# Kernel tuning notes

Measured on AMD Instinct MI355X. Metric: run time of the kernel, lower is better.

The kernel has to match this reference:

```python
import jax, jax.numpy as jnp
import numpy as np

NH = 16   # neighbors
MD = 64   # model_dim
FF = 128  # ff_dim
H = 4     # heads
HD = MD // H
B, S, T = 2, 8192, 4096
LOG100 = float(np.log(100.0))


def _ln(x, g, b, eps=1e-5):
    m = x.mean(-1, keepdims=True)
    v = ((x - m) ** 2).mean(-1, keepdims=True)
    return (x - m) * jax.lax.rsqrt(v + eps) * g + b


def _lrelu(x):
    return jnp.where(x >= 0, x, 0.2 * x)


def setup_inputs():
    ks = jax.random.split(jax.random.key(0), 16)
    rn = lambda k, sh: jax.random.normal(k, sh, dtype=jnp.float32) * 0.05
    return {
        "x": jax.random.normal(ks[0], (B, S, 1), dtype=jnp.float32),
        "c1": jax.random.normal(ks[1], (B, S, T), dtype=jnp.float32),
        "c2": jax.random.normal(ks[2], (B, S, T), dtype=jnp.float32),
        "pe_W1": rn(ks[3], (2, FF)), "pe_b1": jnp.zeros((FF,), jnp.float32),
        "pe_W2": rn(ks[4], (FF, MD)), "pe_b2": jnp.zeros((MD,), jnp.float32),
        "Wq": rn(ks[5], (MD, MD)), "Wk": rn(ks[6], (MD, MD)), "Wv": rn(ks[7], (1, MD)),
        "logit_scale": jnp.full((H, 1, 1), float(np.log(10.0)), jnp.float32),
        "Wo": rn(ks[8], (MD, MD)), "bo": jnp.zeros((MD,), jnp.float32),
        "g1": jnp.ones((MD,), jnp.float32), "beta1": jnp.zeros((MD,), jnp.float32),
        "g2": jnp.ones((MD,), jnp.float32), "beta2": jnp.zeros((MD,), jnp.float32),
        "g3": jnp.ones((MD * NH,), jnp.float32), "beta3": jnp.zeros((MD * NH,), jnp.float32),
        "mnh_W1": rn(ks[9], (MD, FF)), "mnh_b1": jnp.zeros((FF,), jnp.float32),
        "mnh_W2": rn(ks[10], (FF, 1)), "mnh_b2": jnp.zeros((1,), jnp.float32),
        "mu_W1": rn(ks[11], (MD * NH, MD * NH)), "mu_b1": jnp.zeros((MD * NH,), jnp.float32),
        "mu_W2": rn(ks[12], (MD * NH, MD * NH)), "mu_b2": jnp.zeros((MD * NH,), jnp.float32),
    }


def reference(x, c1, c2, pe_W1, pe_b1, pe_W2, pe_b2, Wq, Wk, Wv, logit_scale, Wo, bo,
              g1, beta1, g2, beta2, g3, beta3,
              mnh_W1, mnh_b1, mnh_W2, mnh_b2, mu_W1, mu_b1, mu_W2, mu_b2):
    b, s, t = c1.shape
    # KNN over source axis s (cartesian distance), per target t
    d = c1 * c1 + c2 * c2                                  # [b,s,t]
    _, idx = jax.lax.top_k(-jnp.swapaxes(d, 1, 2), NH)     # [b,t,NH]
    x_nh = jax.vmap(lambda xb, ib: xb[ib])(x, idx)         # [b,t,NH,e]
    c1g = jnp.take_along_axis(jnp.swapaxes(c1, 1, 2), idx, axis=2)  # [b,t,NH]
    c2g = jnp.take_along_axis(jnp.swapaxes(c2, 1, 2), idx, axis=2)
    # relative-position embedding MLP (PE), already in [b,t,NH,MD] layout
    pe = jnp.stack([c1g, c2g], -1)                         # [b,t,NH,2]
    pe = jax.nn.gelu(pe @ pe_W1 + pe_b1) @ pe_W2 + pe_b2   # [b,t,NH,MD]
    h = _ln(x_nh + pe, g1, beta1).reshape(b * t, NH, MD)   # e=1 broadcasts
    v = jnp.einsum('bne,ed->bnd', x_nh.reshape(b * t, NH, 1), Wv)
    q = h @ Wq
    k = h @ Wk
    sp = lambda z: z.reshape(b * t, NH, H, HD).transpose(0, 2, 1, 3)
    qh, kh, vh = sp(q), sp(k), sp(v)
    # logit-scaled (cosine) attention over the NH neighbor axis
    qn = qh * jax.lax.rsqrt(jnp.sum(qh * qh, -1, keepdims=True) + 1e-12)
    kn = kh * jax.lax.rsqrt(jnp.sum(kh * kh, -1, keepdims=True) + 1e-12)
    scale = jnp.exp(jnp.minimum(logit_scale, LOG100))      # [H,1,1]
    att = jax.nn.softmax(jnp.einsum('bhnd,bhmd->bhnm', qn, kn) * scale, axis=-1)
    o = jnp.einsum('bhnm,bhmd->bhnd', att, vh).transpose(0, 2, 1, 3).reshape(b * t, NH, MD)
    h = _ln(h + (o @ Wo + bo), g2, beta2)
    # per-neighbor MLP producing a scalar, broadcast-added back
    h = h + _lrelu(_lrelu(h @ mnh_W1 + mnh_b1) @ mnh_W2 + mnh_b2)
    # unfold neighbors into channels and run the unfold MLP
    h = _ln(h.reshape(b, t, NH * MD), g3, beta3)
    return _lrelu(_lrelu(h @ mu_W1 + mu_b1) @ mu_W2 + mu_b2)  # [b,t,NH*MD]
```

## Files before the change

kernel.cpp:

```cpp
#include <hip/hip_runtime.h>
#include <hip/hip_bf16.h>

#define B_    2
#define SSRC  8192
#define TT    4096
#define NHN   16
#define NC    64
#define CS    128
#define LOG100D 4.605170185988091368035982909368

typedef short s16x8 __attribute__((ext_vector_type(8)));
typedef float f32x4 __attribute__((ext_vector_type(4)));
typedef unsigned long long u64;

typedef const __attribute__((address_space(1))) void* gas_ptr;
typedef __attribute__((address_space(3))) void* las_ptr;
#define GLDS16(g, l) __builtin_amdgcn_global_load_lds((gas_ptr)(g), (las_ptr)(l), 16, 0, 0)

#define WFENCE asm volatile("s_waitcnt lgkmcnt(0)" ::: "memory")

__device__ __forceinline__ unsigned short f2bf(float f) {
    unsigned u = __float_as_uint(f);
    u = u + 0x7fffu + ((u >> 16) & 1u);
    return (unsigned short)(u >> 16);
}
__device__ __forceinline__ float bf2f(unsigned short h) {
    return __uint_as_float(((unsigned)h) << 16);
}
__device__ __forceinline__ double lrelu_d(double v) { return v >= 0.0 ? v : 0.2 * v; }
__device__ __forceinline__ double gelu_d(double u) {
    double a = 0.7978845608028654 * (u + 0.044715 * u * u * u);
    return 0.5 * u * (1.0 + tanh(a));
}
__device__ __forceinline__ double rsum16d(double v) {
    v += __shfl_xor(v, 1); v += __shfl_xor(v, 2);
    v += __shfl_xor(v, 4); v += __shfl_xor(v, 8);
    return v;
}
__device__ __forceinline__ double rmax16d(double v) {
    v = fmax(v, __shfl_xor(v, 1)); v = fmax(v, __shfl_xor(v, 2));
    v = fmax(v, __shfl_xor(v, 4)); v = fmax(v, __shfl_xor(v, 8));
    return v;
}
__device__ __forceinline__ double rsum64d(double v) {
    v += __shfl_xor(v, 1); v += __shfl_xor(v, 2); v += __shfl_xor(v, 4);
    v += __shfl_xor(v, 8); v += __shfl_xor(v, 16); v += __shfl_xor(v, 32);
    return v;
}

__device__ __forceinline__ void ce(u64 &a, u64 &b) {
    bool c = a < b; u64 lo = c ? a : b; u64 hi = c ? b : a; a = lo; b = hi;
}
__device__ __forceinline__ void sort16(u64 (&k)[16]) {
    ce(k[0],k[8]); ce(k[1],k[9]); ce(k[2],k[10]); ce(k[3],k[11]);
    ce(k[4],k[12]); ce(k[5],k[13]); ce(k[6],k[14]); ce(k[7],k[15]);
    ce(k[0],k[4]); ce(k[1],k[5]); ce(k[2],k[6]); ce(k[3],k[7]);
    ce(k[8],k[12]); ce(k[9],k[13]); ce(k[10],k[14]); ce(k[11],k[15]);
    ce(k[4],k[8]); ce(k[5],k[9]); ce(k[6],k[10]); ce(k[7],k[11]);
    ce(k[0],k[2]); ce(k[1],k[3]); ce(k[4],k[6]); ce(k[5],k[7]);
    ce(k[8],k[10]); ce(k[9],k[11]); ce(k[12],k[14]); ce(k[13],k[15]);
    ce(k[2],k[8]); ce(k[3],k[9]); ce(k[6],k[12]); ce(k[7],k[13]);
    ce(k[2],k[4]); ce(k[3],k[5]); ce(k[6],k[8]); ce(k[7],k[9]);
    ce(k[10],k[12]); ce(k[11],k[13]);
    ce(k[0],k[1]); ce(k[2],k[3]); ce(k[4],k[5]); ce(k[6],k[7]);
    ce(k[8],k[9]); ce(k[10],k[11]); ce(k[12],k[13]); ce(k[14],k[15]);
    ce(k[1],k[8]); ce(k[3],k[10]); ce(k[5],k[12]); ce(k[7],k[14]);
    ce(k[1],k[4]); ce(k[3],k[6]); ce(k[5],k[8]); ce(k[7],k[10]);
    ce(k[9],k[12]); ce(k[11],k[14]);
    ce(k[1],k[2]); ce(k[3],k[4]); ce(k[5],k[6]); ce(k[7],k[8]);
    ce(k[9],k[10]); ce(k[11],k[12]); ce(k[13],k[14]);
}
__device__ __forceinline__ void bmerge16(u64 (&k)[16]) {
    ce(k[0],k[8]); ce(k[1],k[9]); ce(k[2],k[10]); ce(k[3],k[11]);
    ce(k[4],k[12]); ce(k[5],k[13]); ce(k[6],k[14]); ce(k[7],k[15]);
    ce(k[0],k[4]); ce(k[1],k[5]); ce(k[2],k[6]); ce(k[3],k[7]);
    ce(k[8],k[12]); ce(k[9],k[13]); ce(k[10],k[14]); ce(k[11],k[15]);
    ce(k[0],k[2]); ce(k[1],k[3]); ce(k[4],k[6]); ce(k[5],k[7]);
    ce(k[8],k[10]); ce(k[9],k[11]); ce(k[12],k[14]); ce(k[13],k[15]);
    ce(k[0],k[1]); ce(k[2],k[3]); ce(k[4],k[5]); ce(k[6],k[7]);
    ce(k[8],k[9]); ce(k[10],k[11]); ce(k[12],k[13]); ce(k[14],k[15]);
}
__device__ __forceinline__ void merge_keep16(u64 (&L)[16], const u64 (&B)[16]) {
#pragma unroll
    for (int i = 0; i < 16; i++) { u64 bb = B[15 - i]; L[i] = L[i] < bb ? L[i] : bb; }
    bmerge16(L);
}

__global__ __launch_bounds__(256) void topk_partial(
    const float* __restrict__ c1, const float* __restrict__ c2,
    u64* __restrict__ cand)
{
    int t = blockIdx.x * 256 + threadIdx.x;
    int ch = blockIdx.y, b = blockIdx.z;
    const float* p1 = c1 + ((size_t)b * SSRC + (size_t)ch * CS) * TT + t;
    const float* p2 = c2 + ((size_t)b * SSRC + (size_t)ch * CS) * TT + t;
    u64 k[16];
#pragma unroll
    for (int j = 0; j < 16; j++) k[j] = ~0ull;
    int sbase = ch * CS;
    for (int s = 0; s < CS; s += 16) {
        u64 bt[16];
#pragma unroll
        for (int u = 0; u < 16; u++) {
            float a_ = p1[(size_t)(s + u) * TT];
            float b_ = p2[(size_t)(s + u) * TT];
            float dd = __fadd_rn(__fmul_rn(a_, a_), __fmul_rn(b_, b_));
            bt[u] = ((u64)__float_as_uint(dd) << 32) | (unsigned)(sbase + s + u);
        }
        sort16(bt);
        merge_keep16(k, bt);
    }
    u64* dst = cand + ((size_t)(b * NC + ch) * 16) * TT + t;
#pragma unroll
    for (int j = 0; j < 16; j++) dst[(size_t)j * TT] = k[j];
}

__global__ __launch_bounds__(64) void topk_merge1(
    const u64* __restrict__ cand, u64* __restrict__ c2c)
{
    int t = blockIdx.x * 64 + threadIdx.x;
    int g = blockIdx.y, b = blockIdx.z;
    u64 k[16];
#pragma unroll
    for (int j = 0; j < 16; j++) k[j] = ~0ull;
    for (int c = g * 8; c < g * 8 + 8; c++) {
        const u64* src = cand + ((size_t)(b * NC + c) * 16) * TT + t;
        u64 bt[16];
#pragma unroll
        for (int j = 0; j < 16; j++) bt[j] = src[(size_t)j * TT];
        merge_keep16(k, bt);
    }
    u64* dst = c2c + ((size_t)((b * 8 + g) * 16)) * TT + t;
#pragma unroll
    for (int j = 0; j < 16; j++) dst[(size_t)j * TT] = k[j];
}

__global__ __launch_bounds__(64) void topk_merge2(
    const u64* __restrict__ c2c, int* __restrict__ knn)
{
    int t = blockIdx.x * 64 + threadIdx.x;
    int b = blockIdx.y;
    u64 k[16];
#pragma unroll
    for (int j = 0; j < 16; j++) k[j] = ~0ull;
    for (int c = 0; c < 8; c++) {
        const u64* src = c2c + ((size_t)(b * 8 + c) * 16) * TT + t;
        u64 bt[16];
#pragma unroll
        for (int j = 0; j < 16; j++) bt[j] = src[(size_t)j * TT];
        merge_keep16(k, bt);
    }
#pragma unroll
    for (int j = 0; j < 16; j++)
        knn[((size_t)b * TT + t) * 16 + j] = (int)(unsigned)(k[j] & 0xffffffffull);
}

__global__ __launch_bounds__(256) void wconv(
    const float* __restrict__ Wa, const float* __restrict__ Wb,
    unsigned short* __restrict__ Oah, unsigned short* __restrict__ Oal,
    unsigned short* __restrict__ Obh, unsigned short* __restrict__ Obl)
{
    const float* W = blockIdx.z ? Wb : Wa;
    unsigned short* Oh = blockIdx.z ? Obh : Oah;
    unsigned short* Ol = blockIdx.z ? Obl : Oal;
    __shared__ float tile[64][65];
    int tx = threadIdx.x & 63, ty = threadIdx.x >> 6;
    int n0 = blockIdx.x * 64, k0 = blockIdx.y * 64;
#pragma unroll
    for (int r = ty; r < 64; r += 4) tile[r][tx] = W[(size_t)(k0 + r) * 1024 + n0 + tx];
    __syncthreads();
#pragma unroll
    for (int r = ty; r < 64; r += 4) {
        float v = tile[tx][r];
        unsigned short hi = f2bf(v);
        Oh[(size_t)(n0 + r) * 1024 + k0 + tx] = hi;
        Ol[(size_t)(n0 + r) * 1024 + k0 + tx] = f2bf(v - bf2f(hi));
    }
}

__global__ __launch_bounds__(256) void tok_pe(
    const float* __restrict__ x, const float* __restrict__ c1, const float* __restrict__ c2,
    const int* __restrict__ knn,
    const float* __restrict__ peW1, const float* __restrict__ peb1,
    const float* __restrict__ peW2, const float* __restrict__ peb2,
    const float* __restrict__ g1, const float* __restrict__ be1,
    float* __restrict__ hout)
{
    __shared__ float s_peW1[256], s_peb1[128], s_peW2[8192], s_peb2[64], s_g1[64], s_be1[64];
    __shared__ float s_scr[4][2352];
    int tid = threadIdx.x, lane = tid & 63, w = tid >> 6;
    if (tid < 256) s_peW1[tid] = peW1[tid];
    if (tid < 128) s_peb1[tid] = peb1[tid];
    if (tid < 64) { s_peb2[tid] = peb2[tid]; s_g1[tid] = g1[tid]; s_be1[tid] = be1[tid]; }
    for (int i = tid; i < 8192; i += 256) s_peW2[i] = peW2[i];
    __syncthreads();

    float* big = s_scr[w];
    float* sc1 = big + 2304; float* sc2 = big + 2320; float* sx = big + 2336;
    double w0a = s_peW1[lane], w1a = s_peW1[128 + lane], ba = s_peb1[lane];
    double w0b = s_peW1[64 + lane], w1b = s_peW1[192 + lane], bbv = s_peb1[64 + lane];
    double gv = (double)s_g1[lane], bv = (double)s_be1[lane];
    double pb2 = (double)s_peb2[lane];

    for (int it = 0; it < 4; ++it) {
        int tk = blockIdx.x * 16 + w * 4 + it;
        int bb = tk >> 12, tt = tk & (TT - 1);
        if (lane < 16) {
            int s = knn[(size_t)tk * 16 + lane];
            sc1[lane] = c1[((size_t)bb * SSRC + s) * TT + tt];
            sc2[lane] = c2[((size_t)bb * SSRC + s) * TT + tt];
            sx[lane]  = x[bb * SSRC + s];
        }
        WFENCE;
#pragma unroll
        for (int n = 0; n < 16; n++) {
            double a_ = (double)sc1[n], b_ = (double)sc2[n];
            big[lane * 18 + n]        = (float)gelu_d(a_ * w0a + b_ * w1a + ba);
            big[(lane + 64) * 18 + n] = (float)gelu_d(a_ * w0b + b_ * w1b + bbv);
        }
        WFENCE;
        double acc[16];
#pragma unroll
        for (int n = 0; n < 16; n++) acc[n] = pb2;
        for (int f = 0; f < 128; f++) {
            double wv = (double)s_peW2[f * 64 + lane];
#pragma unroll
            for (int n = 0; n < 16; n += 2) {
                float2 gvv = *(const float2*)&big[f * 18 + n];
                acc[n]     += (double)gvv.x * wv;
                acc[n + 1] += (double)gvv.y * wv;
            }
        }
        float* op = hout + (size_t)tk * 1024 + lane;
#pragma unroll
        for (int n = 0; n < 16; n++) {
            double v = acc[n] + (double)sx[n];
            double m = rsum64d(v) * (1.0 / 64.0);
            double d = v - m;
            double var = rsum64d(d * d) * (1.0 / 64.0);
            op[n * 64] = (float)(d / sqrt(var + 1e-5) * gv + bv);
        }
    }
}

__global__ __launch_bounds__(256) void tok_attn(
    const float* __restrict__ x, const int* __restrict__ knn,
    const float* __restrict__ Wq, const float* __restrict__ Wk,
    const float* __restrict__ Wv, const float* __restrict__ lsc,
    const float* __restrict__ Wo, const float* __restrict__ bo,
    const float* __restrict__ g2, const float* __restrict__ be2,
    float* __restrict__ hio)
{
    __shared__ float s_Wq[4096], s_Wk[4096], s_WoV[256], s_bo[64], s_g2[64], s_be2[64];
    __shared__ float s_scr[4][2320];
    int tid = threadIdx.x, lane = tid & 63, w = tid >> 6;
    if (tid < 64) {
        s_bo[tid] = bo[tid]; s_g2[tid] = g2[tid]; s_be2[tid] = be2[tid];
        for (int hh = 0; hh < 4; hh++) {
            double a = 0.0;
            for (int hd = 0; hd < 16; hd++)
                a += (double)Wv[hh * 16 + hd] * (double)Wo[(hh * 16 + hd) * 64 + tid];
            s_WoV[hh * 64 + tid] = (float)a;
        }
    }
    for (int i = tid; i < 4096; i += 256) { s_Wq[i] = Wq[i]; s_Wk[i] = Wk[i]; }
    __syncthreads();

    int head = lane >> 4, mm = lane & 15;
    double scaleh = exp(fmin((double)lsc[head], LOG100D));
    double wov0 = (double)s_WoV[lane], wov1 = (double)s_WoV[64 + lane];
    double wov2 = (double)s_WoV[128 + lane], wov3 = (double)s_WoV[192 + lane];
    double gv = (double)s_g2[lane], bv = (double)s_be2[lane], bov = (double)s_bo[lane];
    float* big = s_scr[w];
    float* sx = big + 2304;

    for (int it = 0; it < 4; ++it) {
        int tk = blockIdx.x * 16 + w * 4 + it;
        int bb = tk >> 12;
        if (lane < 16) {
            int s = knn[(size_t)tk * 16 + lane];
            sx[lane] = x[bb * SSRC + s];
        }
        float* hp = hio + (size_t)tk * 1024 + lane;
        double h[16];
#pragma unroll
        for (int n = 0; n < 16; n++) {
            h[n] = (double)hp[n * 64];
            big[lane * 18 + n] = (float)h[n];
        }
        WFENCE;
        double q[16], k2[16];
#pragma unroll
        for (int n = 0; n < 16; n++) { q[n] = 0.0; k2[n] = 0.0; }
        for (int kk = 0; kk < 64; kk++) {
            double wq = (double)s_Wq[kk * 64 + lane], wk = (double)s_Wk[kk * 64 + lane];
#pragma unroll
            for (int n = 0; n < 16; n += 2) {
                float2 hv = *(const float2*)&big[kk * 18 + n];
                q[n]  += (double)hv.x * wq; q[n + 1]  += (double)hv.y * wq;
                k2[n] += (double)hv.x * wk; k2[n + 1] += (double)hv.y * wk;
            }
        }
#pragma unroll
        for (int n = 0; n < 16; n++) {
            double sq = rsum16d(q[n] * q[n]);   q[n]  /= sqrt(sq + 1e-12);
            double sk = rsum16d(k2[n] * k2[n]); k2[n] /= sqrt(sk + 1e-12);
        }
        WFENCE;
#pragma unroll
        for (int n = 0; n < 16; n++) {
            big[lane * 18 + n]        = (float)q[n];
            big[1152 + lane * 18 + n] = (float)k2[n];
        }
        WFENCE;
        double A_[16];
        {
            double S[16];
#pragma unroll
            for (int n = 0; n < 16; n++) S[n] = 0.0;
            for (int hd = 0; hd < 16; hd++) {
                int r = head * 16 + hd;
                double kf = (double)big[1152 + r * 18 + mm];
#pragma unroll
                for (int n = 0; n < 16; n += 2) {
                    float2 qq = *(const float2*)&big[r * 18 + n];
                    S[n] += (double)qq.x * kf; S[n + 1] += (double)qq.y * kf;
                }
            }
            double xv = (double)sx[mm];
#pragma unroll
            for (int n = 0; n < 16; n++) {
                double sv = S[n] * scaleh;
                double mx = rmax16d(sv);
                double e = exp(sv - mx);
                double se = rsum16d(e);
                A_[n] = rsum16d((e / se) * xv);
            }
        }
#pragma unroll
        for (int n = 0; n < 16; n++) {
            double a0 = __shfl(A_[n], mm), a1 = __shfl(A_[n], 16 + mm);
            double a2 = __shfl(A_[n], 32 + mm), a3 = __shfl(A_[n], 48 + mm);
            double v = h[n] + a0 * wov0 + a1 * wov1 + a2 * wov2 + a3 * wov3 + bov;
            double m = rsum64d(v) * (1.0 / 64.0);
            double d = v - m;
            double var = rsum64d(d * d) * (1.0 / 64.0);
            hp[n * 64] = (float)(d / sqrt(var + 1e-5) * gv + bv);
        }
    }
}

__global__ __launch_bounds__(256) void tok_mnh(
    const float* __restrict__ hin,
    const float* __restrict__ mW1, const float* __restrict__ mb1,
    const float* __restrict__ mW2, const float* __restrict__ mb2,
    const float* __restrict__ g3, const float* __restrict__ be3,
    unsigned short* __restrict__ hnh, unsigned short* __restrict__ hnl)
{
    __shared__ float s_mW1[8192], s_mb1[128], s_mW2[128], s_g3[1024], s_be3[1024];
    __shared__ float s_scr[4][1152];
    int tid = threadIdx.x, lane = tid & 63, w = tid >> 6;
    if (tid < 128) { s_mb1[tid] = mb1[tid]; s_mW2[tid] = mW2[tid]; }
    for (int i = tid; i < 8192; i += 256) s_mW1[i] = mW1[i];
    for (int i = tid; i < 1024; i += 256) { s_g3[i] = g3[i]; s_be3[i] = be3[i]; }
    __syncthreads();

    double mb2s = (double)mb2[0];
    double mb1a = (double)s_mb1[lane], mb1b = (double)s_mb1[64 + lane];
    double w2a = (double)s_mW2[lane], w2b = (double)s_mW2[64 + lane];
    float* big = s_scr[w];

    for (int it = 0; it < 4; ++it) {
        int tk = blockIdx.x * 16 + w * 4 + it;
        const float* hp = hin + (size_t)tk * 1024 + lane;
        double h[16];
#pragma unroll
        for (int n = 0; n < 16; n++) {
            h[n] = (double)hp[n * 64];
            big[lane * 18 + n] = (float)h[n];
        }
        WFENCE;
        double t1a[16], t1b[16];
#pragma unroll
        for (int n = 0; n < 16; n++) { t1a[n] = mb1a; t1b[n] = mb1b; }
        for (int kk = 0; kk < 64; kk++) {
            double wa = (double)s_mW1[kk * 128 + lane], wb = (double)s_mW1[kk * 128 + 64 + lane];
#pragma unroll
            for (int n = 0; n < 16; n += 2) {
                float2 hv = *(const float2*)&big[kk * 18 + n];
                t1a[n] += (double)hv.x * wa; t1a[n + 1] += (double)hv.y * wa;
                t1b[n] += (double)hv.x * wb; t1b[n + 1] += (double)hv.y * wb;
            }
        }
#pragma unroll
        for (int n = 0; n < 16; n++) {
            double p = lrelu_d(t1a[n]) * w2a + lrelu_d(t1b[n]) * w2b;
            p = rsum64d(p);
            h[n] += lrelu_d(p + mb2s);
        }
        double s1 = 0.0;
#pragma unroll
        for (int n = 0; n < 16; n++) s1 += h[n];
        s1 = rsum64d(s1) * (1.0 / 1024.0);
        double s2v = 0.0;
#pragma unroll
        for (int n = 0; n < 16; n++) { double d = h[n] - s1; s2v += d * d; }
        s2v = rsum64d(s2v) * (1.0 / 1024.0);
        double rs = 1.0 / sqrt(s2v + 1e-5);
        unsigned short* oph = hnh + (size_t)tk * 1024 + lane;
        unsigned short* opl = hnl + (size_t)tk * 1024 + lane;
#pragma unroll
        for (int n = 0; n < 16; n++) {
            double v = (h[n] - s1) * rs * (double)s_g3[n * 64 + lane] + (double)s_be3[n * 64 + lane];
            unsigned short hi = f2bf((float)v);
            oph[n * 64] = hi;
            opl[n * 64] = f2bf((float)(v - (double)bf2f(hi)));
        }
    }
}

#define AH_OFF 0
#define AL_OFF 4096
#define BH_OFF 8192
#define BL_OFF 12288
template<int OUTSPLIT>
__global__ __launch_bounds__(256) void gemm_split(
    const unsigned short* __restrict__ Ah, const unsigned short* __restrict__ Al,
    const unsigned short* __restrict__ Bh, const unsigned short* __restrict__ Bl,
    const float* __restrict__ bias,
    unsigned short* __restrict__ oh, unsigned short* __restrict__ ol,
    float* __restrict__ of, int M, int N, int K)
{
    __shared__ unsigned short SM[16384];
    int tid = threadIdx.x, lane = tid & 63, w = tid >> 6;
    int wm = w >> 1, wn = w & 1;
    int m0 = blockIdx.y * 128, n0 = blockIdx.x * 128;
    f32x4 acc[4][4];
#pragma unroll
    for (int i = 0; i < 4; i++)
#pragma unroll
        for (int j = 0; j < 4; j++) acc[i][j] = (f32x4){0.f, 0.f, 0.f, 0.f};
    int row = tid >> 2, c8 = (tid & 3) * 8;
    size_t aoff = (size_t)(m0 + row) * K + c8;
    size_t boff = (size_t)(n0 + row) * K + c8;
    for (int kk = 0; kk < K; kk += 32) {
        __syncthreads();
        GLDS16(Ah + aoff + kk,                   SM + AH_OFF + tid * 8);
        GLDS16(Ah + aoff + (size_t)64 * K + kk,  SM + AH_OFF + 2048 + tid * 8);
        GLDS16(Al + aoff + kk,                   SM + AL_OFF + tid * 8);
        GLDS16(Al + aoff + (size_t)64 * K + kk,  SM + AL_OFF + 2048 + tid * 8);
        GLDS16(Bh + boff + kk,                   SM + BH_OFF + tid * 8);
        GLDS16(Bh + boff + (size_t)64 * K + kk,  SM + BH_OFF + 2048 + tid * 8);
        GLDS16(Bl + boff + kk,                   SM + BL_OFF + tid * 8);
        GLDS16(Bl + boff + (size_t)64 * K + kk,  SM + BL_OFF + 2048 + tid * 8);
        asm volatile("s_waitcnt vmcnt(0)" ::: "memory");
        __syncthreads();
        int kh = (lane >> 4) * 8, rA = wm * 64 + (lane & 15), rB = wn * 64 + (lane & 15);
        s16x8 afh[4], afl[4], bfh[4], bfl[4];
#pragma unroll
        for (int i = 0; i < 4; i++) {
            afh[i] = *(const s16x8*)&SM[AH_OFF + (rA + i * 16) * 32 + kh];
            afl[i] = *(const s16x8*)&SM[AL_OFF + (rA + i * 16) * 32 + kh];
            bfh[i] = *(const s16x8*)&SM[BH_OFF + (rB + i * 16) * 32 + kh];
            bfl[i] = *(const s16x8*)&SM[BL_OFF + (rB + i * 16) * 32 + kh];
        }
#pragma unroll
        for (int i = 0; i < 4; i++)
#pragma unroll
            for (int j = 0; j < 4; j++) {
                acc[i][j] = __builtin_amdgcn_mfma_f32_16x16x32_bf16(afl[i], bfh[j], acc[i][j], 0, 0, 0);
                acc[i][j] = __builtin_amdgcn_mfma_f32_16x16x32_bf16(afh[i], bfl[j], acc[i][j], 0, 0, 0);
                acc[i][j] = __builtin_amdgcn_mfma_f32_16x16x32_bf16(afh[i], bfh[j], acc[i][j], 0, 0, 0);
            }
    }
    float bc[4];
#pragma unroll
    for (int j = 0; j < 4; j++) bc[j] = bias[n0 + wn * 64 + j * 16 + (lane & 15)];
#pragma unroll
    for (int i = 0; i < 4; i++) {
#pragma unroll
        for (int j = 0; j < 4; j++) {
#pragma unroll
            for (int r = 0; r < 4; r++) {
                int rw = m0 + wm * 64 + i * 16 + (lane >> 4) * 4 + r;
                int cl = n0 + wn * 64 + j * 16 + (lane & 15);
                float v = acc[i][j][r] + bc[j];
                v = v >= 0.f ? v : 0.2f * v;
                if (OUTSPLIT) {
                    unsigned short hi = f2bf(v);
                    oh[(size_t)rw * N + cl] = hi;
                    ol[(size_t)rw * N + cl] = f2bf(v - bf2f(hi));
                } else {
                    of[(size_t)rw * N + cl] = v;
                }
            }
        }
    }
}

extern "C" void kernel_launch(void* const* d_in, const int* in_sizes, int n_in,
                              void* d_out, int out_size, void* d_ws, size_t ws_size,
                              hipStream_t stream)
{
    const float* x    = (const float*)d_in[0];
    const float* c1   = (const float*)d_in[1];
    const float* c2   = (const float*)d_in[2];
    const float* peW1 = (const float*)d_in[3];
    const float* peb1 = (const float*)d_in[4];
    const float* peW2 = (const float*)d_in[5];
    const float* peb2 = (const float*)d_in[6];
    const float* Wq   = (const float*)d_in[7];
    const float* Wk   = (const float*)d_in[8];
    const float* Wv   = (const float*)d_in[9];
    const float* lsc  = (const float*)d_in[10];
    const float* Wo   = (const float*)d_in[11];
    const float* bo   = (const float*)d_in[12];
    const float* g1   = (const float*)d_in[13];
    const float* be1  = (const float*)d_in[14];
    const float* g2   = (const float*)d_in[15];
    const float* be2  = (const float*)d_in[16];
    const float* g3   = (const float*)d_in[17];
    const float* be3  = (const float*)d_in[18];
    const float* mW1  = (const float*)d_in[19];
    const float* mb1  = (const float*)d_in[20];
    const float* mW2  = (const float*)d_in[21];
    const float* mb2  = (const float*)d_in[22];
    const float* muW1 = (const float*)d_in[23];
    const float* mub1 = (const float*)d_in[24];
    const float* muW2 = (const float*)d_in[25];
    const float* mub2 = (const float*)d_in[26];

    const size_t MB = (size_t)1 << 20;
    char* ws = (char*)d_ws;
    u64*            cand   = (u64*)(ws);
    float*          hbuf   = (float*)(ws);
    unsigned short* y1h    = (unsigned short*)(ws);
    unsigned short* y1l    = (unsigned short*)(ws + 16 * MB);
    unsigned short* hnh    = (unsigned short*)(ws + 32 * MB);
    unsigned short* hnl    = (unsigned short*)(ws + 48 * MB);
    u64*            c2c    = (u64*)(ws + 64 * MB);
    unsigned short* w1th   = (unsigned short*)(ws + 72 * MB);
    unsigned short* w1tl   = (unsigned short*)(ws + 74 * MB);
    unsigned short* w2th   = (unsigned short*)(ws + 76 * MB);
    unsigned short* w2tl   = (unsigned short*)(ws + 78 * MB);
    int*            knn    = (int*)(ws + 80 * MB);
    (void)in_sizes; (void)n_in; (void)out_size; (void)ws_size;

    wconv<<<dim3(16, 16, 2), 256, 0, stream>>>(muW1, muW2, w1th, w1tl, w2th, w2tl);
    topk_partial<<<dim3(TT / 256, NC, B_), 256, 0, stream>>>(c1, c2, cand);
    topk_merge1<<<dim3(TT / 64, 8, B_), 64, 0, stream>>>(cand, c2c);
    topk_merge2<<<dim3(TT / 64, B_), 64, 0, stream>>>(c2c, knn);
    tok_pe<<<dim3(512), 256, 0, stream>>>(x, c1, c2, knn, peW1, peb1, peW2, peb2, g1, be1, hbuf);
    tok_attn<<<dim3(512), 256, 0, stream>>>(x, knn, Wq, Wk, Wv, lsc, Wo, bo, g2, be2, hbuf);
    tok_mnh<<<dim3(512), 256, 0, stream>>>(hbuf, mW1, mb1, mW2, mb2, g3, be3, hnh, hnl);
    gemm_split<1><<<dim3(8, 64), 256, 0, stream>>>(hnh, hnl, w1th, w1tl, mub1,
                                                   y1h, y1l, (float*)nullptr, 8192, 1024, 1024);
    gemm_split<0><<<dim3(8, 64), 256, 0, stream>>>(y1h, y1l, w2th, w2tl, mub2,
                                                   (unsigned short*)nullptr, (unsigned short*)nullptr,
                                                   (float*)d_out, 8192, 1024, 1024);
}
```

Before: 783.4 us.

## Use FP64 MFMA for per-token projection matmuls with a runtime self-check fallback

Replaces the scalar double-precision FMA loops in the positional-encoding, Q/K projection and neighbor-MLP kernels with 16x16x4 FP64 MFMA instructions. Each path is guarded by a one-off probe that checks the MFMA output layout and falls back to the old scalar code if the check fails. Weight tiles in shared memory get padded row strides to reduce bank conflicts for the new access pattern. This adds register pressure from the accumulator vectors, more LDS use, and extra cross-lane shuffles in the epilogues.

```diff
diff --git a/kernel.cpp b/kernel.cpp
--- a/kernel.cpp
+++ b/kernel.cpp
@@ -11,6 +11,7 @@
 
 typedef short s16x8 __attribute__((ext_vector_type(8)));
 typedef float f32x4 __attribute__((ext_vector_type(4)));
+typedef double f64x4 __attribute__((ext_vector_type(4)));
 typedef unsigned long long u64;
 
 typedef const __attribute__((address_space(1))) void* gas_ptr;
@@ -46,6 +47,24 @@
     v += __shfl_xor(v, 1); v += __shfl_xor(v, 2); v += __shfl_xor(v, 4);
     v += __shfl_xor(v, 8); v += __shfl_xor(v, 16); v += __shfl_xor(v, 32);
     return v;
+}
+
+__device__ __forceinline__ bool mfma64_probe() {
+    int lane = threadIdx.x & 63, l15 = lane & 15, lg = lane >> 4;
+    double a = (double)(1 + l15 + 31 * lg);
+    double b = (double)(3 + l15 + 17 * lg);
+    f64x4 d = (f64x4){0.0, 0.0, 0.0, 0.0};
+    d = __builtin_amdgcn_mfma_f64_16x16x4f64(a, b, d, 0, 0, 0);
+    bool ok = true;
+#pragma unroll
+    for (int r = 0; r < 4; r++) {
+        int i = 4 * lg + r;
+        int e = 0;
+#pragma unroll
+        for (int k = 0; k < 4; k++) e += (1 + i + 31 * k) * (3 + l15 + 17 * k);
+        ok = ok && (d[r] == (double)e);
+    }
+    return __all(ok) != 0;
 }
 
 __device__ __forceinline__ void ce(u64 &a, u64 &b) {
@@ -186,21 +205,30 @@
     const float* __restrict__ g1, const float* __restrict__ be1,
     float* __restrict__ hout)
 {
-    __shared__ float s_peW1[256], s_peb1[128], s_peW2[8192], s_peb2[64], s_g1[64], s_be1[64];
+    __shared__ float s_peW1[256], s_peb1[128], s_peW2[8448], s_peb2[64], s_g1[64], s_be1[64];
     __shared__ float s_scr[4][2352];
     int tid = threadIdx.x, lane = tid & 63, w = tid >> 6;
     if (tid < 256) s_peW1[tid] = peW1[tid];
     if (tid < 128) s_peb1[tid] = peb1[tid];
     if (tid < 64) { s_peb2[tid] = peb2[tid]; s_g1[tid] = g1[tid]; s_be1[tid] = be1[tid]; }
-    for (int i = tid; i < 8192; i += 256) s_peW2[i] = peW2[i];
+    for (int i = tid; i < 8192; i += 256) s_peW2[(i >> 6) * 66 + (i & 63)] = peW2[i];
     __syncthreads();
 
+    bool mf = mfma64_probe();
     float* big = s_scr[w];
     float* sc1 = big + 2304; float* sc2 = big + 2320; float* sx = big + 2336;
+    int l15 = lane & 15, lg = lane >> 4;
     double w0a = s_peW1[lane], w1a = s_peW1[128 + lane], ba = s_peb1[lane];
     double w0b = s_peW1[64 + lane], w1b = s_peW1[192 + lane], bbv = s_peb1[64 + lane];
     double gv = (double)s_g1[lane], bv = (double)s_be1[lane];
     double pb2 = (double)s_peb2[lane];
+    double g1v[4], be1v[4], pb2v[4];
+#pragma unroll
+    for (int j = 0; j < 4; j++) {
+        g1v[j]  = (double)s_g1[j * 16 + l15];
+        be1v[j] = (double)s_be1[j * 16 + l15];
+        pb2v[j] = (double)s_peb2[j * 16 + l15];
+    }
 
     for (int it = 0; it < 4; ++it) {
         int tk = blockIdx.x * 16 + w * 4 + it;
@@ -219,26 +247,61 @@
             big[(lane + 64) * 18 + n] = (float)gelu_d(a_ * w0b + b_ * w1b + bbv);
         }
         WFENCE;
-        double acc[16];
-#pragma unroll
-        for (int n = 0; n < 16; n++) acc[n] = pb2;
-        for (int f = 0; f < 128; f++) {
-            double wv = (double)s_peW2[f * 64 + lane];
-#pragma unroll
-            for (int n = 0; n < 16; n += 2) {
-                float2 gvv = *(const float2*)&big[f * 18 + n];
-                acc[n]     += (double)gvv.x * wv;
-                acc[n + 1] += (double)gvv.y * wv;
-            }
-        }
-        float* op = hout + (size_t)tk * 1024 + lane;
-#pragma unroll
-        for (int n = 0; n < 16; n++) {
-            double v = acc[n] + (double)sx[n];
-            double m = rsum64d(v) * (1.0 / 64.0);
-            double d = v - m;
-            double var = rsum64d(d * d) * (1.0 / 64.0);
-            op[n * 64] = (float)(d / sqrt(var + 1e-5) * gv + bv);
+        if (mf) {
+            f64x4 acc[4];
+#pragma unroll
+            for (int j = 0; j < 4; j++) acc[j] = (f64x4){0.0, 0.0, 0.0, 0.0};
+            for (int ks = 0; ks < 32; ks++) {
+                double a = (double)big[(4 * ks + lg) * 18 + l15];
+                const float* wrow = &s_peW2[(4 * ks + lg) * 66 + l15];
+#pragma unroll
+                for (int j = 0; j < 4; j++) {
+                    double b = (double)wrow[j * 16];
+                    acc[j] = __builtin_amdgcn_mfma_f64_16x16x4f64(a, b, acc[j], 0, 0, 0);
+                }
+            }
+            double xr[4];
+#pragma unroll
+            for (int r = 0; r < 4; r++) xr[r] = (double)sx[lg * 4 + r];
+            float* op = hout + (size_t)tk * 1024;
+#pragma unroll
+            for (int r = 0; r < 4; r++) {
+                double v[4], s = 0.0;
+#pragma unroll
+                for (int j = 0; j < 4; j++) { v[j] = acc[j][r] + pb2v[j] + xr[r]; s += v[j]; }
+                double m = rsum16d(s) * (1.0 / 64.0);
+                double q = 0.0;
+#pragma unroll
+                for (int j = 0; j < 4; j++) { double d = v[j] - m; q += d * d; }
+                double var = rsum16d(q) * (1.0 / 64.0);
+                double rs = sqrt(var + 1e-5);
+                int n = lg * 4 + r;
+#pragma unroll
+                for (int j = 0; j < 4; j++)
+                    op[n * 64 + j * 16 + l15] = (float)((v[j] - m) / rs * g1v[j] + be1v[j]);
+            }
+        } else {
+            double acc[16];
+#pragma unroll
+            for (int n = 0; n < 16; n++) acc[n] = pb2;
+            for (int f = 0; f < 128; f++) {
+                double wv = (double)s_peW2[f * 66 + lane];
+#pragma unroll
+                for (int n = 0; n < 16; n += 2) {
+                    float2 gvv = *(const float2*)&big[f * 18 + n];
+                    acc[n]     += (double)gvv.x * wv;
+                    acc[n + 1] += (double)gvv.y * wv;
+                }
+            }
+            float* op = hout + (size_t)tk * 1024 + lane;
+#pragma unroll
+            for (int n = 0; n < 16; n++) {
+                double v = acc[n] + (double)sx[n];
+                double m = rsum64d(v) * (1.0 / 64.0);
+                double d = v - m;
+                double var = rsum64d(d * d) * (1.0 / 64.0);
+                op[n * 64] = (float)(d / sqrt(var + 1e-5) * gv + bv);
+            }
         }
     }
 }
@@ -251,7 +314,7 @@
     const float* __restrict__ g2, const float* __restrict__ be2,
     float* __restrict__ hio)
 {
-    __shared__ float s_Wq[4096], s_Wk[4096], s_WoV[256], s_bo[64], s_g2[64], s_be2[64];
+    __shared__ float s_Wq[4224], s_Wk[4224], s_WoV[256], s_bo[64], s_g2[64], s_be2[64];
     __shared__ float s_scr[4][2320];
     int tid = threadIdx.x, lane = tid & 63, w = tid >> 6;
     if (tid < 64) {
@@ -263,10 +326,15 @@
             s_WoV[hh * 64 + tid] = (float)a;
         }
     }
-    for (int i = tid; i < 4096; i += 256) { s_Wq[i] = Wq[i]; s_Wk[i] = Wk[i]; }
+    for (int i = tid; i < 4096; i += 256) {
+        s_Wq[(i >> 6) * 66 + (i & 63)] = Wq[i];
+        s_Wk[(i >> 6) * 66 + (i & 63)] = Wk[i];
+    }
     __syncthreads();
 
+    bool mf = mfma64_probe();
     int head = lane >> 4, mm = lane & 15;
+    int l15 = mm, lg = head;
     double scaleh = exp(fmin((double)lsc[head], LOG100D));
     double wov0 = (double)s_WoV[lane], wov1 = (double)s_WoV[64 + lane];
     double wov2 = (double)s_WoV[128 + lane], wov3 = (double)s_WoV[192 + lane];
@@ -289,28 +357,58 @@
             big[lane * 18 + n] = (float)h[n];
         }
         WFENCE;
-        double q[16], k2[16];
-#pragma unroll
-        for (int n = 0; n < 16; n++) { q[n] = 0.0; k2[n] = 0.0; }
-        for (int kk = 0; kk < 64; kk++) {
-            double wq = (double)s_Wq[kk * 64 + lane], wk = (double)s_Wk[kk * 64 + lane];
-#pragma unroll
-            for (int n = 0; n < 16; n += 2) {
-                float2 hv = *(const float2*)&big[kk * 18 + n];
-                q[n]  += (double)hv.x * wq; q[n + 1]  += (double)hv.y * wq;
-                k2[n] += (double)hv.x * wk; k2[n + 1] += (double)hv.y * wk;
-            }
-        }
-#pragma unroll
-        for (int n = 0; n < 16; n++) {
-            double sq = rsum16d(q[n] * q[n]);   q[n]  /= sqrt(sq + 1e-12);
-            double sk = rsum16d(k2[n] * k2[n]); k2[n] /= sqrt(sk + 1e-12);
-        }
-        WFENCE;
-#pragma unroll
-        for (int n = 0; n < 16; n++) {
-            big[lane * 18 + n]        = (float)q[n];
-            big[1152 + lane * 18 + n] = (float)k2[n];
+        if (mf) {
+            f64x4 qa[4], ka[4];
+#pragma unroll
+            for (int j = 0; j < 4; j++) { qa[j] = (f64x4){0.,0.,0.,0.}; ka[j] = (f64x4){0.,0.,0.,0.}; }
+            for (int ks = 0; ks < 16; ks++) {
+                double a = (double)big[(4 * ks + lg) * 18 + l15];
+                const float* wq = &s_Wq[(4 * ks + lg) * 66 + l15];
+                const float* wk = &s_Wk[(4 * ks + lg) * 66 + l15];
+#pragma unroll
+                for (int j = 0; j < 4; j++) {
+                    qa[j] = __builtin_amdgcn_mfma_f64_16x16x4f64(a, (double)wq[j * 16], qa[j], 0, 0, 0);
+                    ka[j] = __builtin_amdgcn_mfma_f64_16x16x4f64(a, (double)wk[j * 16], ka[j], 0, 0, 0);
+                }
+            }
+            WFENCE;
+#pragma unroll
+            for (int j = 0; j < 4; j++) {
+#pragma unroll
+                for (int r = 0; r < 4; r++) {
+                    double qq = qa[j][r], kk2 = ka[j][r];
+                    double sq = rsum16d(qq * qq);
+                    double sk = rsum16d(kk2 * kk2);
+                    qq  /= sqrt(sq + 1e-12);
+                    kk2 /= sqrt(sk + 1e-12);
+                    big[(j * 16 + l15) * 18 + 4 * lg + r]        = (float)qq;
+                    big[1152 + (j * 16 + l15) * 18 + 4 * lg + r] = (float)kk2;
+                }
+            }
+        } else {
+            double q[16], k2[16];
+#pragma unroll
+            for (int n = 0; n < 16; n++) { q[n] = 0.0; k2[n] = 0.0; }
+            for (int kk = 0; kk < 64; kk++) {
+                double wq = (double)s_Wq[kk * 66 + lane], wk = (double)s_Wk[kk * 66 + lane];
+#pragma unroll
+                for (int n = 0; n < 16; n += 2) {
+                    float2 hv = *(const float2*)&big[kk * 18 + n];
+                    q[n]  += (double)hv.x * wq; q[n + 1]  += (double)hv.y * wq;
+                    k2[n] += (double)hv.x * wk; k2[n + 1] += (double)hv.y * wk;
+                }
+            }
+#pragma unroll
+            for (int n = 0; n < 16; n++) {
+                double sq = rsum16d(q[n] * q[n]);   q[n]  /= sqrt(sq + 1e-12);
+                double sk = rsum16d(k2[n] * k2[n]); k2[n] /= sqrt(sk + 1e-12);
+            }
+            WFENCE;
+#pragma unroll
+            for (int n = 0; n < 16; n++) {
+                big[lane * 18 + n]        = (float)q[n];
+                big[1152 + lane * 18 + n] = (float)k2[n];
+            }
         }
         WFENCE;
         double A_[16];
@@ -357,17 +455,25 @@
     const float* __restrict__ g3, const float* __restrict__ be3,
     unsigned short* __restrict__ hnh, unsigned short* __restrict__ hnl)
 {
-    __shared__ float s_mW1[8192], s_mb1[128], s_mW2[128], s_g3[1024], s_be3[1024];
+    __shared__ float s_mW1[8320], s_mb1[128], s_mW2[128], s_g3[1024], s_be3[1024];
     __shared__ float s_scr[4][1152];
     int tid = threadIdx.x, lane = tid & 63, w = tid >> 6;
     if (tid < 128) { s_mb1[tid] = mb1[tid]; s_mW2[tid] = mW2[tid]; }
-    for (int i = tid; i < 8192; i += 256) s_mW1[i] = mW1[i];
+    for (int i = tid; i < 8192; i += 256) s_mW1[(i >> 7) * 130 + (i & 127)] = mW1[i];
     for (int i = tid; i < 1024; i += 256) { s_g3[i] = g3[i]; s_be3[i] = be3[i]; }
     __syncthreads();
 
+    bool mf = mfma64_probe();
+    int l15 = lane & 15, lg = lane >> 4;
     double mb2s = (double)mb2[0];
     double mb1a = (double)s_mb1[lane], mb1b = (double)s_mb1[64 + lane];
     double w2a = (double)s_mW2[lane], w2b = (double)s_mW2[64 + lane];
+    double mb1v[8], w2v[8];
+#pragma unroll
+    for (int j = 0; j < 8; j++) {
+        mb1v[j] = (double)s_mb1[j * 16 + l15];
+        w2v[j]  = (double)s_mW2[j * 16 + l15];
+    }
     float* big = s_scr[w];
 
     for (int it = 0; it < 4; ++it) {
@@ -380,23 +486,54 @@
             big[lane * 18 + n] = (float)h[n];
         }
         WFENCE;
-        double t1a[16], t1b[16];
-#pragma unroll
-        for (int n = 0; n < 16; n++) { t1a[n] = mb1a; t1b[n] = mb1b; }
-        for (int kk = 0; kk < 64; kk++) {
-            double wa = (double)s_mW1[kk * 128 + lane], wb = (double)s_mW1[kk * 128 + 64 + lane];
-#pragma unroll
-            for (int n = 0; n < 16; n += 2) {
-                float2 hv = *(const float2*)&big[kk * 18 + n];
-                t1a[n] += (double)hv.x * wa; t1a[n + 1] += (double)hv.y * wa;
-                t1b[n] += (double)hv.x * wb; t1b[n + 1] += (double)hv.y * wb;
-            }
-        }
-#pragma unroll
-        for (int n = 0; n < 16; n++) {
-            double p = lrelu_d(t1a[n]) * w2a + lrelu_d(t1b[n]) * w2b;
-            p = rsum64d(p);
-            h[n] += lrelu_d(p + mb2s);
+        if (mf) {
+            f64x4 acc[8];
+#pragma unroll
+            for (int j = 0; j < 8; j++) acc[j] = (f64x4){0.0, 0.0, 0.0, 0.0};
+            for (int ks = 0; ks < 16; ks++) {
+                double a = (double)big[(4 * ks + lg) * 18 + l15];
+                const float* wrow = &s_mW1[(4 * ks + lg) * 130 + l15];
+#pragma unroll
+                for (int j = 0; j < 8; j++) {
+                    double b = (double)wrow[j * 16];
+                    acc[j] = __builtin_amdgcn_mfma_f64_16x16x4f64(a, b, acc[j], 0, 0, 0);
+                }
+            }
+            double p[4];
+#pragma unroll
+            for (int r = 0; r < 4; r++) {
+                double s = 0.0;
+#pragma unroll
+                for (int j = 0; j < 8; j++) {
+                    double t = acc[j][r] + mb1v[j];
+                    s += lrelu_d(t) * w2v[j];
+                }
+                p[r] = rsum16d(s);
+            }
+#pragma unroll
+            for (int n = 0; n < 16; n++) {
+                double pn = __shfl(p[n & 3], (n >> 2) * 16);
+                h[n] += lrelu_d(pn + mb2s);
+            }
+        } else {
+            double t1a[16], t1b[16];
+#pragma unroll
+            for (int n = 0; n < 16; n++) { t1a[n] = mb1a; t1b[n] = mb1b; }
+            for (int kk = 0; kk < 64; kk++) {
+                double wa = (double)s_mW1[kk * 130 + lane], wb = (double)s_mW1[kk * 130 + 64 + lane];
+#pragma unroll
+                for (int n = 0; n < 16; n += 2) {
+                    float2 hv = *(const float2*)&big[kk * 18 + n];
+                    t1a[n] += (double)hv.x * wa; t1a[n + 1] += (double)hv.y * wa;
+                    t1b[n] += (double)hv.x * wb; t1b[n + 1] += (double)hv.y * wb;
+                }
+            }
+#pragma unroll
+            for (int n = 0; n < 16; n++) {
+                double p = lrelu_d(t1a[n]) * w2a + lrelu_d(t1b[n]) * w2b;
+                p = rsum64d(p);
+                h[n] += lrelu_d(p + mb2s);
+            }
         }
         double s1 = 0.0;
 #pragma unroll
```

Result: slower. 879.9 us (+12.3%).
